# Kernel tuning notes

Hardware: AMD Instinct MI355X
Metric: run time of the kernel (lower is better)

Reference implementation:

```python
import jax, jax.numpy as jnp
import numpy as np

FRAMES = 4
SLICE = 14
BATCH = 4
NODES = 2 * FRAMES * SLICE * SLICE  # 1568
C = 2048
LN_EPS = 1e-5


def _layer(x, w, g, b):
    # Linear(no bias) -> LayerNorm(2048) -> LeakyReLU(0.1)
    y = jnp.einsum('bnc,dc->bnd', x, w)
    m = jnp.mean(y, axis=-1, keepdims=True)
    v = jnp.mean((y - m) ** 2, axis=-1, keepdims=True)
    y = (y - m) / jnp.sqrt(v + LN_EPS) * g + b
    return jax.nn.leaky_relu(y, 0.1)


def setup_inputs() -> dict:
    key = jax.random.key(0)
    ks = jax.random.split(key, 8)
    w = lambda k, sh: (jax.random.normal(k, sh, jnp.float32) * 0.02)
    return {
        'x': jax.random.normal(ks[0], (BATCH, NODES, C), jnp.float32),
        'w_fc1': w(ks[1], (C, C)),
        'w1': w(ks[2], (C, C)), 'g1': jnp.ones((C,), jnp.float32), 'b1': jnp.zeros((C,), jnp.float32),
        'w2': w(ks[3], (C, C)), 'g2': jnp.ones((C,), jnp.float32), 'b2': jnp.zeros((C,), jnp.float32),
        'w3': w(ks[4], (C, C)), 'g3': jnp.ones((C,), jnp.float32), 'b3': jnp.zeros((C,), jnp.float32),
        'conv1_w': w(ks[5], (2 * FRAMES,)),            # Conv2d(2F->1, k=1) weight squeezed
        'conv1_b': jnp.zeros((1,), jnp.float32),
        'deconv_w': w(ks[6], (C, 1024, 3, 3)),          # ConvTranspose2d weight [in, out, kH, kW]
        'deconv_b': jnp.zeros((1024,), jnp.float32),
    }


def reference(x, w_fc1, w1, g1, b1, w2, g2, b2, w3, g3, b3, conv1_w, conv1_b, deconv_w, deconv_b):
    # ---- adjacency_laplacian ----
    h = jnp.einsum('bnc,dc->bnd', x, w_fc1)                 # fc1
    s = jnp.einsum('bnd,bmd->bnm', h, h)                    # out @ out^T
    sq = s * s
    adj = sq / jnp.sum(sq, axis=1, keepdims=True)           # square_normalize (sum over dim=1)
    adj = adj + jnp.eye(NODES, dtype=adj.dtype)             # A + I
    d = 1.0 / jnp.sqrt(jnp.sum(adj, axis=1))                # [B, n]
    # D^{-1/2} A D^{-1/2}: diag matmuls are exactly row/col scaling
    lap = d[:, :, None] * adj * d[:, None, :]

    # ---- graph-conv stack ----
    out = jnp.matmul(lap, x)
    out = _layer(out, w1, g1, b1)
    out = jnp.matmul(lap, out)
    out = _layer(out, w2, g2, b2)
    out = jnp.matmul(lap, out)
    out = _layer(out, w3, g3, b3)

    # ---- head: transpose, reshape, 1x1 conv over 2F frame-channels ----
    out = jnp.swapaxes(out, 1, 2)                           # [B, 2048, nodes]
    out = out.reshape(BATCH * C, 2 * FRAMES, SLICE, SLICE)
    out = jnp.einsum('nfhw,f->nhw', out, conv1_w) + conv1_b[0]
    out = out.reshape(BATCH, C, SLICE, SLICE)

    # bilinear upsample x2 (align_corners=False == half-pixel, matches jax.image.resize)
    out = jax.image.resize(out, (BATCH, C, 2 * SLICE, 2 * SLICE), method='bilinear')

    # ConvTranspose2d(2048->1024, k=3, pad=1, stride=3) as dilated conv with flipped kernel
    wk = jnp.flip(deconv_w, axis=(-2, -1)).transpose(1, 0, 2, 3)  # [out, in, 3, 3]
    out = jax.lax.conv_general_dilated(
        out, wk, window_strides=(1, 1), padding=((1, 1), (1, 1)),
        lhs_dilation=(3, 3), dimension_numbers=('NCHW', 'OIHW', 'NCHW'))
    out = out + deconv_b[None, :, None, None]               # [B, 1024, 82, 82]
    return out
```

## Files before the change

### kernel.cpp

```cpp
#include <hip/hip_runtime.h>

typedef __bf16 bf16;
typedef __bf16 bf16x4 __attribute__((ext_vector_type(4)));
typedef __bf16 bf16x8 __attribute__((ext_vector_type(8)));
typedef float f32x4 __attribute__((ext_vector_type(4)));

#define N_NODES 1568
#define CDIM 2048

__device__ __forceinline__ void async_copy16(const bf16* g, bf16* l) {
    __builtin_amdgcn_global_load_lds(
        (const __attribute__((address_space(1))) unsigned int*)g,
        (__attribute__((address_space(3))) unsigned int*)l, 16, 0, 0);
}

template <typename OUT_T>
__global__ __launch_bounds__(512, 2) void gemm256_nt(const bf16* __restrict__ A,
                                                     const bf16* __restrict__ B,
                                                     OUT_T* __restrict__ C,
                                                     int M, int N, int K) {
    __shared__ __align__(16) bf16 lds[2][2][256 * 64];
    const int m0 = blockIdx.x * 256, n0 = blockIdx.y * 256;
    const int t = threadIdx.x;
    const int lane = t & 63, wave = t >> 6;
    const int wm = wave >> 2, wn = wave & 3;
    const int l15 = lane & 15, quad = lane >> 4, rx7 = l15 & 7;

    const int cg = (((t & 7) ^ ((t >> 3) & 7)) << 3);
    const int rb = t >> 3;
    const bf16* ga[4];
    const bf16* gb[4];
#pragma unroll
    for (int i = 0; i < 4; i++) {
        int ra = m0 + rb + i * 64; if (ra >= M) ra = M - 1;
        int rn = n0 + rb + i * 64; if (rn >= N) rn = N - 1;
        ga[i] = A + (long)ra * K + cg;
        gb[i] = B + (long)rn * K + cg;
    }
    const int ldst = t * 8;

    f32x4 acc[8][4];
#pragma unroll
    for (int i = 0; i < 8; i++)
#pragma unroll
        for (int j = 0; j < 4; j++) acc[i][j] = (f32x4){0.f, 0.f, 0.f, 0.f};

    auto stage = [&](int buf, int k0) {
        bf16* sAx = &lds[buf][0][0];
        bf16* sBx = &lds[buf][1][0];
#pragma unroll
        for (int i = 0; i < 4; i++)
            async_copy16(ga[i] + k0, sAx + ldst + i * 4096);
#pragma unroll
        for (int i = 0; i < 4; i++)
            async_copy16(gb[i] + k0, sBx + ldst + i * 4096);
    };

    const int NT = K >> 6;
    stage(0, 0);
    stage(1, 64);
    asm volatile("s_waitcnt vmcnt(8)" ::: "memory");
    __builtin_amdgcn_s_barrier();

    bf16x8 bfr[4][2], afr[2][2];
    for (int tt = 0; tt < NT; ++tt) {
        const bf16* sA = &lds[tt & 1][0][0];
        const bf16* sB = &lds[tt & 1][1][0];

        auto rdB = [&]() {
#pragma unroll
            for (int nf = 0; nf < 4; ++nf)
#pragma unroll
                for (int kk = 0; kk < 2; ++kk)
                    bfr[nf][kk] = *(const bf16x8*)(sB + (wn * 64 + nf * 16 + l15) * 64 +
                                                   ((((kk << 2) | quad) ^ rx7) << 3));
        };
        auto rdA = [&](int q) {
#pragma unroll
            for (int mi = 0; mi < 2; ++mi)
#pragma unroll
                for (int kk = 0; kk < 2; ++kk)
                    afr[mi][kk] = *(const bf16x8*)(sA + (wm * 128 + (q * 2 + mi) * 16 + l15) * 64 +
                                                   ((((kk << 2) | quad) ^ rx7) << 3));
        };
        auto mfq = [&](int q) {
            __builtin_amdgcn_s_setprio(1);
#pragma unroll
            for (int kk = 0; kk < 2; ++kk)
#pragma unroll
                for (int mi = 0; mi < 2; ++mi)
#pragma unroll
                    for (int nf = 0; nf < 4; ++nf)
                        acc[q * 2 + mi][nf] = __builtin_amdgcn_mfma_f32_16x16x32_bf16(
                            afr[mi][kk], bfr[nf][kk], acc[q * 2 + mi][nf], 0, 0, 0);
            __builtin_amdgcn_s_setprio(0);
        };

        rdB();
        rdA(0); mfq(0);
        rdA(1); mfq(1);
        rdA(2); mfq(2);
        rdA(3);
        asm volatile("s_waitcnt lgkmcnt(0)" ::: "memory");
        __builtin_amdgcn_s_barrier();
        if (tt + 2 < NT) stage(tt & 1, (tt + 2) << 6);
        mfq(3);
        if (tt + 2 < NT) { asm volatile("s_waitcnt vmcnt(8)" ::: "memory"); }
        else             { asm volatile("s_waitcnt vmcnt(0)" ::: "memory"); }
        __builtin_amdgcn_s_barrier();
    }

#pragma unroll
    for (int mf = 0; mf < 8; ++mf) {
        const int row0 = m0 + wm * 128 + mf * 16 + quad * 4;
#pragma unroll
        for (int nf = 0; nf < 4; ++nf) {
            const int col = n0 + wn * 64 + nf * 16 + l15;
            if (col < N) {
#pragma unroll
                for (int r = 0; r < 4; ++r) {
                    const int row = row0 + r;
                    if (row < M) C[(long)row * N + col] = (OUT_T)acc[mf][nf][r];
                }
            }
        }
    }
}

template <typename OUT_T>
__global__ __launch_bounds__(256, 2) void gemm_nt(const bf16* __restrict__ A,
                                                  const bf16* __restrict__ B,
                                                  OUT_T* __restrict__ C,
                                                  int M, int N, int K,
                                                  long sAb, long sBb, long sCb) {
    __shared__ __align__(16) bf16 sA[128 * 32];
    __shared__ __align__(16) bf16 sB[128 * 32];
    const int bz = blockIdx.z;
    A += (long)bz * sAb; B += (long)bz * sBb; C += (long)bz * sCb;
    const int m0 = blockIdx.x * 128, n0 = blockIdx.y * 128;
    const int t = threadIdx.x;
    const int lane = t & 63, wave = t >> 6;
    const int wr = wave >> 1, wc = wave & 1;
    const int l15 = lane & 15, quad = lane >> 4;

    f32x4 acc[4][4];
#pragma unroll
    for (int i = 0; i < 4; i++)
#pragma unroll
        for (int j = 0; j < 4; j++) acc[i][j] = (f32x4){0.f, 0.f, 0.f, 0.f};

    const int ko = (t & 3) * 8;
    int ra1 = m0 + (t >> 2);          if (ra1 >= M) ra1 = M - 1;
    int ra2 = m0 + ((t + 256) >> 2);  if (ra2 >= M) ra2 = M - 1;
    int rb1 = n0 + (t >> 2);          if (rb1 >= N) rb1 = N - 1;
    int rb2 = n0 + ((t + 256) >> 2);  if (rb2 >= N) rb2 = N - 1;
    const bf16* gA1 = A + (long)ra1 * K + ko;
    const bf16* gA2 = A + (long)ra2 * K + ko;
    const bf16* gB1 = B + (long)rb1 * K + ko;
    const bf16* gB2 = B + (long)rb2 * K + ko;
    bf16* lA1 = sA + t * 8;  bf16* lA2 = sA + (t + 256) * 8;
    bf16* lB1 = sB + t * 8;  bf16* lB2 = sB + (t + 256) * 8;

    for (int k0 = 0; k0 < K; k0 += 32) {
        __syncthreads();
        async_copy16(gA1 + k0, lA1);
        async_copy16(gA2 + k0, lA2);
        async_copy16(gB1 + k0, lB1);
        async_copy16(gB2 + k0, lB2);
        __syncthreads();
        bf16x8 af[4], bfr[4];
#pragma unroll
        for (int i = 0; i < 4; i++)
            af[i] = *(const bf16x8*)(sA + (wr * 64 + i * 16 + l15) * 32 + quad * 8);
#pragma unroll
        for (int j = 0; j < 4; j++)
            bfr[j] = *(const bf16x8*)(sB + (wc * 64 + j * 16 + l15) * 32 + quad * 8);
#pragma unroll
        for (int i = 0; i < 4; i++)
#pragma unroll
            for (int j = 0; j < 4; j++)
                acc[i][j] = __builtin_amdgcn_mfma_f32_16x16x32_bf16(af[i], bfr[j], acc[i][j], 0, 0, 0);
    }
#pragma unroll
    for (int i = 0; i < 4; i++) {
        const int row0 = m0 + wr * 64 + i * 16 + quad * 4;
#pragma unroll
        for (int j = 0; j < 4; j++) {
            const int col = n0 + wc * 64 + j * 16 + l15;
            if (col < N) {
#pragma unroll
                for (int r = 0; r < 4; r++) {
                    const int row = row0 + r;
                    if (row < M) C[(long)row * N + col] = (OUT_T)acc[i][j][r];
                }
            }
        }
    }
}

__global__ __launch_bounds__(256, 2) void gemm_nt_sym(const bf16* __restrict__ A,
                                                      float* __restrict__ C,
                                                      int M, int K,
                                                      long sAb, long sCb) {
    __shared__ __align__(16) bf16 sA[128 * 32];
    __shared__ __align__(16) bf16 sB[128 * 32];
    const int bz = blockIdx.z;
    A += (long)bz * sAb; C += (long)bz * sCb;
    int rem = blockIdx.x, bi = 0;
    while (rem >= 13 - bi) { rem -= 13 - bi; bi++; }
    const int bj = bi + rem;
    const int m0 = bi * 128, n0 = bj * 128;
    const int t = threadIdx.x;
    const int lane = t & 63, wave = t >> 6;
    const int wr = wave >> 1, wc = wave & 1;
    const int l15 = lane & 15, quad = lane >> 4;

    f32x4 acc[4][4];
#pragma unroll
    for (int i = 0; i < 4; i++)
#pragma unroll
        for (int j = 0; j < 4; j++) acc[i][j] = (f32x4){0.f, 0.f, 0.f, 0.f};

    const int ko = (t & 3) * 8;
    int ra1 = m0 + (t >> 2);          if (ra1 >= M) ra1 = M - 1;
    int ra2 = m0 + ((t + 256) >> 2);  if (ra2 >= M) ra2 = M - 1;
    int rb1 = n0 + (t >> 2);          if (rb1 >= M) rb1 = M - 1;
    int rb2 = n0 + ((t + 256) >> 2);  if (rb2 >= M) rb2 = M - 1;
    const bf16* gA1 = A + (long)ra1 * K + ko;
    const bf16* gA2 = A + (long)ra2 * K + ko;
    const bf16* gB1 = A + (long)rb1 * K + ko;
    const bf16* gB2 = A + (long)rb2 * K + ko;
    bf16* lA1 = sA + t * 8;  bf16* lA2 = sA + (t + 256) * 8;
    bf16* lB1 = sB + t * 8;  bf16* lB2 = sB + (t + 256) * 8;

    for (int k0 = 0; k0 < K; k0 += 32) {
        __syncthreads();
        async_copy16(gA1 + k0, lA1);
        async_copy16(gA2 + k0, lA2);
        async_copy16(gB1 + k0, lB1);
        async_copy16(gB2 + k0, lB2);
        __syncthreads();
        bf16x8 af[4], bfr[4];
#pragma unroll
        for (int i = 0; i < 4; i++)
            af[i] = *(const bf16x8*)(sA + (wr * 64 + i * 16 + l15) * 32 + quad * 8);
#pragma unroll
        for (int j = 0; j < 4; j++)
            bfr[j] = *(const bf16x8*)(sB + (wc * 64 + j * 16 + l15) * 32 + quad * 8);
#pragma unroll
        for (int i = 0; i < 4; i++)
#pragma unroll
            for (int j = 0; j < 4; j++)
                acc[i][j] = __builtin_amdgcn_mfma_f32_16x16x32_bf16(af[i], bfr[j], acc[i][j], 0, 0, 0);
    }
    const bool mirror = (bi != bj);
#pragma unroll
    for (int i = 0; i < 4; i++) {
        const int row0 = m0 + wr * 64 + i * 16 + quad * 4;
#pragma unroll
        for (int j = 0; j < 4; j++) {
            const int col = n0 + wc * 64 + j * 16 + l15;
            if (col < M) {
#pragma unroll
                for (int r = 0; r < 4; r++) {
                    const int row = row0 + r;
                    if (row < M) {
                        const float v = acc[i][j][r];
                        C[(long)row * M + col] = v;
                        if (mirror) C[(long)col * M + row] = v;
                    }
                }
            }
        }
    }
}

__global__ __launch_bounds__(256) void cast_f32_bf16_k(const float* __restrict__ in,
                                                       bf16* __restrict__ out, long n) {
    long i = ((long)blockIdx.x * 256 + threadIdx.x) * 4;
    if (i >= n) return;
    float4 v = *(const float4*)(in + i);
    bf16x4 o;
    o[0] = (bf16)v.x; o[1] = (bf16)v.y; o[2] = (bf16)v.z; o[3] = (bf16)v.w;
    *(bf16x4*)(out + i) = o;
}

__global__ __launch_bounds__(256) void cast4_f32_bf16_k(const float* __restrict__ a,
                                                        const float* __restrict__ b,
                                                        const float* __restrict__ c,
                                                        const float* __restrict__ d,
                                                        bf16* __restrict__ out, long n) {
    const int w = blockIdx.y;
    const float* in = (w == 0) ? a : (w == 1) ? b : (w == 2) ? c : d;
    bf16* o = out + (long)w * n;
    long i = ((long)blockIdx.x * 256 + threadIdx.x) * 4;
    if (i >= n) return;
    float4 v = *(const float4*)(in + i);
    bf16x4 ov;
    ov[0] = (bf16)v.x; ov[1] = (bf16)v.y; ov[2] = (bf16)v.z; ov[3] = (bf16)v.w;
    *(bf16x4*)(o + i) = ov;
}

__global__ __launch_bounds__(256) void transpose_bf16_k(const bf16* __restrict__ in,
                                                        bf16* __restrict__ out,
                                                        int R, int C, long sIn, long sOut) {
    __shared__ bf16 tile[64][65];
    in += (long)blockIdx.z * sIn;
    out += (long)blockIdx.z * sOut;
    const int r0 = blockIdx.y * 64, c0 = blockIdx.x * 64;
    const int tx = threadIdx.x & 63, ty = threadIdx.x >> 6;
#pragma unroll
    for (int i = 0; i < 16; i++) {
        int r = ty * 16 + i;
        int gr = r0 + r, gc = c0 + tx;
        tile[r][tx] = (gr < R && gc < C) ? in[(long)gr * C + gc] : (bf16)0.f;
    }
    __syncthreads();
#pragma unroll
    for (int i = 0; i < 16; i++) {
        int c = ty * 16 + i;
        int gc = c0 + c, gr = r0 + tx;
        if (gc < C && gr < R) out[(long)gc * R + gr] = tile[tx][c];
    }
}

__global__ __launch_bounds__(256) void colsum_part_k(const float* __restrict__ s,
                                                     float* __restrict__ part) {
    int m = blockIdx.x * 256 + threadIdx.x;
    if (m >= N_NODES) return;
    int y = blockIdx.y, b = blockIdx.z;
    const float* sb = s + (long)b * N_NODES * N_NODES;
    float acc = 0.f;
    for (int n = y * 196; n < y * 196 + 196; ++n) {
        float v = sb[(long)n * N_NODES + m];
        acc += v * v;
    }
    part[((long)y * 4 + b) * N_NODES + m] = acc;
}

__global__ __launch_bounds__(256) void colsum_comb_k(const float* __restrict__ part,
                                                     float* __restrict__ inv) {
    int m = blockIdx.x * 256 + threadIdx.x;
    if (m >= N_NODES) return;
    int b = blockIdx.y;
    float a = 0.f;
#pragma unroll
    for (int y = 0; y < 8; y++) a += part[((long)y * 4 + b) * N_NODES + m];
    inv[(long)b * N_NODES + m] = 1.0f / a;
}

__global__ __launch_bounds__(256) void lap_build_k(const float* __restrict__ s,
                                                   const float* __restrict__ inv,
                                                   bf16* __restrict__ lap) {
    int m = blockIdx.x * 256 + threadIdx.x;
    if (m >= N_NODES) return;
    int n = blockIdx.y, b = blockIdx.z;
    long off = (long)b * N_NODES * N_NODES + (long)n * N_NODES + m;
    float v = s[off];
    float l = 0.5f * v * v * inv[(long)b * N_NODES + m];
    if (n == m) l += 0.5f;
    lap[off] = (bf16)l;
}

__global__ __launch_bounds__(256) void ln_leaky_k(const float* __restrict__ y,
                                                  const float* __restrict__ g,
                                                  const float* __restrict__ beta,
                                                  bf16* __restrict__ z) {
    const long row = blockIdx.x;
    const float* yr = y + row * CDIM;
    const int t = threadIdx.x;
    float v[8];
    float s = 0.f, ss = 0.f;
#pragma unroll
    for (int i = 0; i < 8; i++) {
        float x = yr[t + 256 * i];
        v[i] = x; s += x; ss += x * x;
    }
#pragma unroll
    for (int o = 32; o > 0; o >>= 1) {
        s += __shfl_down(s, o);
        ss += __shfl_down(ss, o);
    }
    __shared__ float sh[8];
    const int wave = t >> 6;
    if ((t & 63) == 0) { sh[wave] = s; sh[wave + 4] = ss; }
    __syncthreads();
    if (t == 0) {
        float a = 0.f, b2 = 0.f;
#pragma unroll
        for (int w = 0; w < 4; w++) { a += sh[w]; b2 += sh[w + 4]; }
        sh[0] = a; sh[4] = b2;
    }
    __syncthreads();
    const float mean = sh[0] * (1.f / 2048.f);
    const float var = sh[4] * (1.f / 2048.f) - mean * mean;
    const float invs = rsqrtf(var + 1e-5f);
    bf16* zr = z + row * CDIM;
#pragma unroll
    for (int i = 0; i < 8; i++) {
        int c = t + 256 * i;
        float o = (v[i] - mean) * invs * g[c] + beta[c];
        o = o > 0.f ? o : 0.1f * o;
        zr[c] = (bf16)o;
    }
}

__global__ __launch_bounds__(256) void conv1_k(const bf16* __restrict__ z,
                                               const float* __restrict__ cw,
                                               const float* __restrict__ cb,
                                               bf16* __restrict__ tb) {
    const int b = blockIdx.z, hw = blockIdx.y;
    const int c = blockIdx.x * 256 + threadIdx.x;
    float acc = cb[0];
#pragma unroll
    for (int f = 0; f < 8; f++)
        acc += (float)z[((long)b * N_NODES + f * 196 + hw) * CDIM + c] * cw[f];
    tb[((long)b * 196 + hw) * CDIM + c] = (bf16)acc;
}

__global__ __launch_bounds__(256) void upsample_k(const bf16* __restrict__ tb,
                                                  bf16* __restrict__ u) {
    const int b = blockIdx.z, i = blockIdx.y, j = blockIdx.x;
    const float si = 0.5f * i - 0.25f, sj = 0.5f * j - 0.25f;
    const int i0 = (int)floorf(si), j0 = (int)floorf(sj);
    const float wi = si - i0, wj = sj - j0;
    const int i0c = max(i0, 0), i1c = min(i0 + 1, 13);
    const int j0c = max(j0, 0), j1c = min(j0 + 1, 13);
    const bf16* base = tb + (long)b * 196 * CDIM;
    const long r00 = ((long)i0c * 14 + j0c) * CDIM, r01 = ((long)i0c * 14 + j1c) * CDIM;
    const long r10 = ((long)i1c * 14 + j0c) * CDIM, r11 = ((long)i1c * 14 + j1c) * CDIM;
    bf16* ur = u + ((long)(b * 28 + i) * 28 + j) * CDIM;
    const float w00 = (1.f - wi) * (1.f - wj), w01 = (1.f - wi) * wj;
    const float w10 = wi * (1.f - wj), w11 = wi * wj;
    for (int k = 0; k < 8; k++) {
        int cc = threadIdx.x + 256 * k;
        float v = w00 * (float)base[r00 + cc] + w01 * (float)base[r01 + cc] +
                  w10 * (float)base[r10 + cc] + w11 * (float)base[r11 + cc];
        ur[cc] = (bf16)v;
    }
}

__global__ __launch_bounds__(256) void wt_k(const float* __restrict__ dw,
                                            bf16* __restrict__ Wt) {
    const int ic = blockIdx.x * 256 + threadIdx.x;
    const int oc = blockIdx.y;
    const float* src = dw + ((long)ic * 1024 + oc) * 9;
#pragma unroll
    for (int r = 0; r < 3; r++)
#pragma unroll
        for (int s = 0; s < 3; s++) {
            int kh = 2 - r, kw = 2 - s;
            Wt[((long)(kh * 3 + kw) * 1024 + oc) * 2048 + ic] = (bf16)src[r * 3 + s];
        }
}

__global__ __launch_bounds__(256) void deconv_scatter_k(const bf16* __restrict__ r,
                                                        const float* __restrict__ db,
                                                        float* __restrict__ out) {
    const int blk = blockIdx.x;
    const int b = blk >> 10, oc = blk & 1023;
    const float bias = db[oc];
    float* ob = out + (long)blk * 82 * 82;
    for (int e = threadIdx.x; e < 82 * 82; e += 256) {
        const int oh = e / 82, ow = e - oh * 82;
        const int mh = oh % 3, mw = ow % 3;
        const int kh = (mh == 0) ? 1 : ((mh == 1) ? 0 : 2);
        const int kw = (mw == 0) ? 1 : ((mw == 1) ? 0 : 2);
        const int ih = (oh - (1 - kh)) / 3;
        const int iw = (ow - (1 - kw)) / 3;
        const int g = kh * 3 + kw;
        ob[e] = (float)r[(long)(g * 1024 + oc) * 3136 + b * 784 + ih * 28 + iw] + bias;
    }
}

extern "C" void kernel_launch(void* const* d_in, const int* in_sizes, int n_in,
                              void* d_out, int out_size, void* d_ws, size_t ws_size,
                              hipStream_t stream) {
    const float* x        = (const float*)d_in[0];
    const float* w_fc1    = (const float*)d_in[1];
    const float* w1       = (const float*)d_in[2];
    const float* g1       = (const float*)d_in[3];
    const float* b1       = (const float*)d_in[4];
    const float* w2       = (const float*)d_in[5];
    const float* g2       = (const float*)d_in[6];
    const float* b2       = (const float*)d_in[7];
    const float* w3       = (const float*)d_in[8];
    const float* g3       = (const float*)d_in[9];
    const float* b3       = (const float*)d_in[10];
    const float* conv1_w  = (const float*)d_in[11];
    const float* conv1_b  = (const float*)d_in[12];
    const float* deconv_w = (const float*)d_in[13];
    const float* deconv_b = (const float*)d_in[14];
    float* out = (float*)d_out;

    char* W = (char*)d_ws;
    bf16* wb   = (bf16*)(W + 0);
    bf16* xb   = (bf16*)(W + 33554432);
    bf16* xbT  = (bf16*)(W + 59244544);
    bf16* hb   = (bf16*)(W + 84934656);
    bf16* lap  = (bf16*)(W + 110624768);
    bf16* tbuf = (bf16*)(W + 130293760);
    bf16* ubuf = (bf16*)(W + 133505024);
    bf16* Wt   = (bf16*)(W + 146350080);
    float* ybuf = (float*)(W + 184098816);
    float* sbuf = (float*)(W + 184098816);
    float* part = (float*)(W + 235479040);
    float* invc = (float*)(W + 235679744);
    bf16* rbuf = (bf16*)(W + 0);
    bf16* zb = xb;
    bf16* zT = xbT;
    bf16* outN = hb;

    const long WMAT = (long)2048 * 2048;
    bf16* wb0 = wb, *wb1 = wb + WMAT, *wb2 = wb + 2 * WMAT, *wb3 = wb + 3 * WMAT;

    cast4_f32_bf16_k<<<dim3(4096, 4), 256, 0, stream>>>(w_fc1, w1, w2, w3, wb, WMAT);
    cast_f32_bf16_k<<<dim3(12544), 256, 0, stream>>>(x, xb, (long)6272 * 2048);
    wt_k<<<dim3(8, 1024), 256, 0, stream>>>(deconv_w, Wt);

    transpose_bf16_k<<<dim3(32, 25, 4), 256, 0, stream>>>(
        xb, xbT, N_NODES, CDIM, (long)N_NODES * CDIM, (long)N_NODES * CDIM);

    gemm256_nt<bf16><<<dim3(25, 8), 512, 0, stream>>>(xb, wb0, hb, 6272, 2048, 2048);

    gemm_nt_sym<<<dim3(91, 1, 4), 256, 0, stream>>>(
        hb, sbuf, N_NODES, 2048,
        (long)N_NODES * 2048, (long)N_NODES * N_NODES);

    colsum_part_k<<<dim3(7, 8, 4), 256, 0, stream>>>(sbuf, part);
    colsum_comb_k<<<dim3(7, 4), 256, 0, stream>>>(part, invc);
    lap_build_k<<<dim3(7, N_NODES, 4), 256, 0, stream>>>(sbuf, invc, lap);

    const bf16* wlayer[3] = {wb1, wb2, wb3};
    const float* gl[3] = {g1, g2, g3};
    const float* bl[3] = {b1, b2, b3};
    for (int i = 0; i < 3; i++) {
        const bf16* prevT = (i == 0) ? xbT : zT;
        gemm_nt<bf16><<<dim3(13, 16, 4), 256, 0, stream>>>(
            lap, prevT, outN, N_NODES, CDIM, N_NODES,
            (long)N_NODES * N_NODES, (long)CDIM * N_NODES, (long)N_NODES * CDIM);
        gemm256_nt<float><<<dim3(25, 8), 512, 0, stream>>>(
            outN, wlayer[i], ybuf, 6272, 2048, 2048);
        ln_leaky_k<<<dim3(6272), 256, 0, stream>>>(ybuf, gl[i], bl[i], zb);
        if (i < 2) {
            transpose_bf16_k<<<dim3(32, 25, 4), 256, 0, stream>>>(
                zb, zT, N_NODES, CDIM, (long)N_NODES * CDIM, (long)N_NODES * CDIM);
        }
    }

    conv1_k<<<dim3(8, 196, 4), 256, 0, stream>>>(zb, conv1_w, conv1_b, tbuf);
    upsample_k<<<dim3(28, 28, 4), 256, 0, stream>>>(tbuf, ubuf);
    gemm256_nt<bf16><<<dim3(36, 13), 512, 0, stream>>>(Wt, ubuf, rbuf, 9216, 3136, 2048);
    deconv_scatter_k<<<dim3(4096), 256, 0, stream>>>(rbuf, deconv_b, out);

    (void)in_sizes; (void)n_in; (void)out_size; (void)ws_size;
}
```

Before: 1.177 ms.

## Re-pipeline 256-tile GEMM and use it for batched Laplacian and symmetric GEMMs

Restructures the 256x256 GEMM main loop so the async global-to-LDS copies are issued in half-tile pieces interleaved with the four MFMA quarters, with a barrier around each quarter. The kernel gains batch strides, and the old 128-tile gemm_nt and gemm_nt_sym kernels are replaced by 256-tile versions. To fit the 64-wide K tiling, the Laplacian and the transposed activations are zero-padded along K to 1664, and workspace offsets are adjusted to match. The goal is more reuse per tile and better copy/compute overlap for the graph-conv and similarity GEMMs. The cost is extra barriers, fewer and larger blocks on small batched problems, and some wasted work on the padding.

```diff
diff --git a/kernel.cpp b/kernel.cpp
--- a/kernel.cpp
+++ b/kernel.cpp
@@ -7,6 +7,7 @@
 
 #define N_NODES 1568
 #define CDIM 2048
+#define LAP_K 1664
 
 __device__ __forceinline__ void async_copy16(const bf16* g, bf16* l) {
     __builtin_amdgcn_global_load_lds(
@@ -18,8 +19,11 @@
 __global__ __launch_bounds__(512, 2) void gemm256_nt(const bf16* __restrict__ A,
                                                      const bf16* __restrict__ B,
                                                      OUT_T* __restrict__ C,
-                                                     int M, int N, int K) {
+                                                     int M, int N, int K,
+                                                     long sAb, long sBb, long sCb) {
     __shared__ __align__(16) bf16 lds[2][2][256 * 64];
+    const int bz = blockIdx.z;
+    A += (long)bz * sAb; B += (long)bz * sBb; C += (long)bz * sCb;
     const int m0 = blockIdx.x * 256, n0 = blockIdx.y * 256;
     const int t = threadIdx.x;
     const int lane = t & 63, wave = t >> 6;
@@ -38,6 +42,24 @@
         gb[i] = B + (long)rn * K + cg;
     }
     const int ldst = t * 8;
+    const int NT = K >> 6, NI = NT >> 1;
+
+    auto stageA = [&](int buf, int h, int tt) {
+        const int k0 = (tt < NT) ? (tt << 6) : 0;
+        bf16* s = &lds[buf][0][0] + ldst;
+        async_copy16(ga[2 * h] + k0,     s + (2 * h) * 4096);
+        async_copy16(ga[2 * h + 1] + k0, s + (2 * h + 1) * 4096);
+    };
+    auto stageB = [&](int buf, int h, int tt) {
+        const int k0 = (tt < NT) ? (tt << 6) : 0;
+        bf16* s = &lds[buf][1][0] + ldst;
+        async_copy16(gb[2 * h] + k0,     s + (2 * h) * 4096);
+        async_copy16(gb[2 * h + 1] + k0, s + (2 * h + 1) * 4096);
+    };
+
+    stageA(0, 0, 0); stageA(0, 1, 0);
+    stageB(0, 0, 0); stageB(0, 1, 0);
+    stageB(1, 0, 1); stageB(1, 1, 1);
 
     f32x4 acc[8][4];
 #pragma unroll
@@ -45,70 +67,58 @@
 #pragma unroll
         for (int j = 0; j < 4; j++) acc[i][j] = (f32x4){0.f, 0.f, 0.f, 0.f};
 
-    auto stage = [&](int buf, int k0) {
-        bf16* sAx = &lds[buf][0][0];
-        bf16* sBx = &lds[buf][1][0];
-#pragma unroll
-        for (int i = 0; i < 4; i++)
-            async_copy16(ga[i] + k0, sAx + ldst + i * 4096);
-#pragma unroll
-        for (int i = 0; i < 4; i++)
-            async_copy16(gb[i] + k0, sBx + ldst + i * 4096);
-    };
-
-    const int NT = K >> 6;
-    stage(0, 0);
-    stage(1, 64);
-    asm volatile("s_waitcnt vmcnt(8)" ::: "memory");
+    asm volatile("s_waitcnt vmcnt(4)" ::: "memory");
     __builtin_amdgcn_s_barrier();
 
     bf16x8 bfr[4][2], afr[2][2];
-    for (int tt = 0; tt < NT; ++tt) {
-        const bf16* sA = &lds[tt & 1][0][0];
-        const bf16* sB = &lds[tt & 1][1][0];
-
-        auto rdB = [&]() {
-#pragma unroll
-            for (int nf = 0; nf < 4; ++nf)
-#pragma unroll
-                for (int kk = 0; kk < 2; ++kk)
-                    bfr[nf][kk] = *(const bf16x8*)(sB + (wn * 64 + nf * 16 + l15) * 64 +
-                                                   ((((kk << 2) | quad) ^ rx7) << 3));
-        };
-        auto rdA = [&](int q) {
+    auto rdB = [&](int cb) {
+        const bf16* sB = &lds[cb][1][0];
+#pragma unroll
+        for (int nf = 0; nf < 4; ++nf)
+#pragma unroll
+            for (int kk = 0; kk < 2; ++kk)
+                bfr[nf][kk] = *(const bf16x8*)(sB + (wn * 64 + nf * 16 + l15) * 64 +
+                                               ((((kk << 2) | quad) ^ rx7) << 3));
+    };
+    auto rdA = [&](int cb, int q) {
+        const bf16* sA = &lds[cb][0][0];
+#pragma unroll
+        for (int mi = 0; mi < 2; ++mi)
+#pragma unroll
+            for (int kk = 0; kk < 2; ++kk)
+                afr[mi][kk] = *(const bf16x8*)(sA + (wm * 128 + (q * 2 + mi) * 16 + l15) * 64 +
+                                               ((((kk << 2) | quad) ^ rx7) << 3));
+    };
+    auto sync_mfma = [&](int q, bool vm) {
+        __builtin_amdgcn_s_barrier();
+        asm volatile("s_waitcnt lgkmcnt(0)" ::: "memory");
+        __builtin_amdgcn_sched_barrier(0);
+        __builtin_amdgcn_s_setprio(1);
+#pragma unroll
+        for (int kk = 0; kk < 2; ++kk)
 #pragma unroll
             for (int mi = 0; mi < 2; ++mi)
 #pragma unroll
-                for (int kk = 0; kk < 2; ++kk)
-                    afr[mi][kk] = *(const bf16x8*)(sA + (wm * 128 + (q * 2 + mi) * 16 + l15) * 64 +
-                                                   ((((kk << 2) | quad) ^ rx7) << 3));
-        };
-        auto mfq = [&](int q) {
-            __builtin_amdgcn_s_setprio(1);
-#pragma unroll
-            for (int kk = 0; kk < 2; ++kk)
-#pragma unroll
-                for (int mi = 0; mi < 2; ++mi)
-#pragma unroll
-                    for (int nf = 0; nf < 4; ++nf)
-                        acc[q * 2 + mi][nf] = __builtin_amdgcn_mfma_f32_16x16x32_bf16(
-                            afr[mi][kk], bfr[nf][kk], acc[q * 2 + mi][nf], 0, 0, 0);
-            __builtin_amdgcn_s_setprio(0);
-        };
-
-        rdB();
-        rdA(0); mfq(0);
-        rdA(1); mfq(1);
-        rdA(2); mfq(2);
-        rdA(3);
-        asm volatile("s_waitcnt lgkmcnt(0)" ::: "memory");
+                for (int nf = 0; nf < 4; ++nf)
+                    acc[q * 2 + mi][nf] = __builtin_amdgcn_mfma_f32_16x16x32_bf16(
+                        afr[mi][kk], bfr[nf][kk], acc[q * 2 + mi][nf], 0, 0, 0);
+        __builtin_amdgcn_s_setprio(0);
+        if (vm) asm volatile("s_waitcnt vmcnt(4)" ::: "memory");
         __builtin_amdgcn_s_barrier();
-        if (tt + 2 < NT) stage(tt & 1, (tt + 2) << 6);
-        mfq(3);
-        if (tt + 2 < NT) { asm volatile("s_waitcnt vmcnt(8)" ::: "memory"); }
-        else             { asm volatile("s_waitcnt vmcnt(0)" ::: "memory"); }
-        __builtin_amdgcn_s_barrier();
-    }
+    };
+
+    for (int j = 0; j < NI; ++j) {
+        const int t0 = 2 * j;
+        rdB(0); rdA(0, 0); stageA(1, 0, t0 + 1); sync_mfma(0, false);
+        rdA(0, 1);         stageA(1, 1, t0 + 1); sync_mfma(1, false);
+        rdA(0, 2);         stageB(0, 0, t0 + 2); sync_mfma(2, false);
+        rdA(0, 3);         stageB(0, 1, t0 + 2); sync_mfma(3, true);
+        rdB(1); rdA(1, 0); stageA(0, 0, t0 + 2); sync_mfma(0, false);
+        rdA(1, 1);         stageA(0, 1, t0 + 2); sync_mfma(1, false);
+        rdA(1, 2);         stageB(1, 0, t0 + 3); sync_mfma(2, false);
+        rdA(1, 3);         stageB(1, 1, t0 + 3); sync_mfma(3, true);
+    }
+    asm volatile("s_waitcnt vmcnt(0)" ::: "memory");
 
 #pragma unroll
     for (int mf = 0; mf < 8; ++mf) {
@@ -127,145 +137,126 @@
     }
 }
 
-template <typename OUT_T>
-__global__ __launch_bounds__(256, 2) void gemm_nt(const bf16* __restrict__ A,
-                                                  const bf16* __restrict__ B,
-                                                  OUT_T* __restrict__ C,
-                                                  int M, int N, int K,
-                                                  long sAb, long sBb, long sCb) {
-    __shared__ __align__(16) bf16 sA[128 * 32];
-    __shared__ __align__(16) bf16 sB[128 * 32];
-    const int bz = blockIdx.z;
-    A += (long)bz * sAb; B += (long)bz * sBb; C += (long)bz * sCb;
-    const int m0 = blockIdx.x * 128, n0 = blockIdx.y * 128;
-    const int t = threadIdx.x;
-    const int lane = t & 63, wave = t >> 6;
-    const int wr = wave >> 1, wc = wave & 1;
-    const int l15 = lane & 15, quad = lane >> 4;
-
-    f32x4 acc[4][4];
-#pragma unroll
-    for (int i = 0; i < 4; i++)
-#pragma unroll
-        for (int j = 0; j < 4; j++) acc[i][j] = (f32x4){0.f, 0.f, 0.f, 0.f};
-
-    const int ko = (t & 3) * 8;
-    int ra1 = m0 + (t >> 2);          if (ra1 >= M) ra1 = M - 1;
-    int ra2 = m0 + ((t + 256) >> 2);  if (ra2 >= M) ra2 = M - 1;
-    int rb1 = n0 + (t >> 2);          if (rb1 >= N) rb1 = N - 1;
-    int rb2 = n0 + ((t + 256) >> 2);  if (rb2 >= N) rb2 = N - 1;
-    const bf16* gA1 = A + (long)ra1 * K + ko;
-    const bf16* gA2 = A + (long)ra2 * K + ko;
-    const bf16* gB1 = B + (long)rb1 * K + ko;
-    const bf16* gB2 = B + (long)rb2 * K + ko;
-    bf16* lA1 = sA + t * 8;  bf16* lA2 = sA + (t + 256) * 8;
-    bf16* lB1 = sB + t * 8;  bf16* lB2 = sB + (t + 256) * 8;
-
-    for (int k0 = 0; k0 < K; k0 += 32) {
-        __syncthreads();
-        async_copy16(gA1 + k0, lA1);
-        async_copy16(gA2 + k0, lA2);
-        async_copy16(gB1 + k0, lB1);
-        async_copy16(gB2 + k0, lB2);
-        __syncthreads();
-        bf16x8 af[4], bfr[4];
-#pragma unroll
-        for (int i = 0; i < 4; i++)
-            af[i] = *(const bf16x8*)(sA + (wr * 64 + i * 16 + l15) * 32 + quad * 8);
-#pragma unroll
-        for (int j = 0; j < 4; j++)
-            bfr[j] = *(const bf16x8*)(sB + (wc * 64 + j * 16 + l15) * 32 + quad * 8);
-#pragma unroll
-        for (int i = 0; i < 4; i++)
-#pragma unroll
-            for (int j = 0; j < 4; j++)
-                acc[i][j] = __builtin_amdgcn_mfma_f32_16x16x32_bf16(af[i], bfr[j], acc[i][j], 0, 0, 0);
-    }
-#pragma unroll
-    for (int i = 0; i < 4; i++) {
-        const int row0 = m0 + wr * 64 + i * 16 + quad * 4;
-#pragma unroll
-        for (int j = 0; j < 4; j++) {
-            const int col = n0 + wc * 64 + j * 16 + l15;
-            if (col < N) {
-#pragma unroll
-                for (int r = 0; r < 4; r++) {
-                    const int row = row0 + r;
-                    if (row < M) C[(long)row * N + col] = (OUT_T)acc[i][j][r];
-                }
-            }
-        }
-    }
-}
-
-__global__ __launch_bounds__(256, 2) void gemm_nt_sym(const bf16* __restrict__ A,
+__global__ __launch_bounds__(512, 2) void gemm256_sym(const bf16* __restrict__ A,
                                                       float* __restrict__ C,
                                                       int M, int K,
                                                       long sAb, long sCb) {
-    __shared__ __align__(16) bf16 sA[128 * 32];
-    __shared__ __align__(16) bf16 sB[128 * 32];
+    __shared__ __align__(16) bf16 lds[2][2][256 * 64];
     const int bz = blockIdx.z;
     A += (long)bz * sAb; C += (long)bz * sCb;
+    const int side = (M + 255) >> 8;
     int rem = blockIdx.x, bi = 0;
-    while (rem >= 13 - bi) { rem -= 13 - bi; bi++; }
+    while (rem >= side - bi) { rem -= side - bi; bi++; }
     const int bj = bi + rem;
-    const int m0 = bi * 128, n0 = bj * 128;
+    const int m0 = bi * 256, n0 = bj * 256;
     const int t = threadIdx.x;
     const int lane = t & 63, wave = t >> 6;
-    const int wr = wave >> 1, wc = wave & 1;
-    const int l15 = lane & 15, quad = lane >> 4;
-
-    f32x4 acc[4][4];
-#pragma unroll
-    for (int i = 0; i < 4; i++)
+    const int wm = wave >> 2, wn = wave & 3;
+    const int l15 = lane & 15, quad = lane >> 4, rx7 = l15 & 7;
+
+    const int cg = (((t & 7) ^ ((t >> 3) & 7)) << 3);
+    const int rb = t >> 3;
+    const bf16* ga[4];
+    const bf16* gb[4];
+#pragma unroll
+    for (int i = 0; i < 4; i++) {
+        int ra = m0 + rb + i * 64; if (ra >= M) ra = M - 1;
+        int rn = n0 + rb + i * 64; if (rn >= M) rn = M - 1;
+        ga[i] = A + (long)ra * K + cg;
+        gb[i] = A + (long)rn * K + cg;
+    }
+    const int ldst = t * 8;
+    const int NT = K >> 6, NI = NT >> 1;
+
+    auto stageA = [&](int buf, int h, int tt) {
+        const int k0 = (tt < NT) ? (tt << 6) : 0;
+        bf16* s = &lds[buf][0][0] + ldst;
+        async_copy16(ga[2 * h] + k0,     s + (2 * h) * 4096);
+        async_copy16(ga[2 * h + 1] + k0, s + (2 * h + 1) * 4096);
+    };
+    auto stageB = [&](int buf, int h, int tt) {
+        const int k0 = (tt < NT) ? (tt << 6) : 0;
+        bf16* s = &lds[buf][1][0] + ldst;
+        async_copy16(gb[2 * h] + k0,     s + (2 * h) * 4096);
+        async_copy16(gb[2 * h + 1] + k0, s + (2 * h + 1) * 4096);
+    };
+
+    stageA(0, 0, 0); stageA(0, 1, 0);
+    stageB(0, 0, 0); stageB(0, 1, 0);
+    stageB(1, 0, 1); stageB(1, 1, 1);
+
+    f32x4 acc[8][4];
+#pragma unroll
+    for (int i = 0; i < 8; i++)
 #pragma unroll
         for (int j = 0; j < 4; j++) acc[i][j] = (f32x4){0.f, 0.f, 0.f, 0.f};
 
-    const int ko = (t & 3) * 8;
-    int ra1 = m0 + (t >> 2);          if (ra1 >= M) ra1 = M - 1;
-    int ra2 = m0 + ((t + 256) >> 2);  if (ra2 >= M) ra2 = M - 1;
-    int rb1 = n0 + (t >> 2);          if (rb1 >= M) rb1 = M - 1;
-    int rb2 = n0 + ((t + 256) >> 2);  if (rb2 >= M) rb2 = M - 1;
-    const bf16* gA1 = A + (long)ra1 * K + ko;
-    const bf16* gA2 = A + (long)ra2 * K + ko;
-    const bf16* gB1 = A + (long)rb1 * K + ko;
-    const bf16* gB2 = A + (long)rb2 * K + ko;
-    bf16* lA1 = sA + t * 8;  bf16* lA2 = sA + (t + 256) * 8;
-    bf16* lB1 = sB + t * 8;  bf16* lB2 = sB + (t + 256) * 8;
-
-    for (int k0 = 0; k0 < K; k0 += 32) {
-        __syncthreads();
-        async_copy16(gA1 + k0, lA1);
-        async_copy16(gA2 + k0, lA2);
-        async_copy16(gB1 + k0, lB1);
-        async_copy16(gB2 + k0, lB2);
-        __syncthreads();
-        bf16x8 af[4], bfr[4];
-#pragma unroll
-        for (int i = 0; i < 4; i++)
-            af[i] = *(const bf16x8*)(sA + (wr * 64 + i * 16 + l15) * 32 + quad * 8);
-#pragma unroll
-        for (int j = 0; j < 4; j++)
-            bfr[j] = *(const bf16x8*)(sB + (wc * 64 + j * 16 + l15) * 32 + quad * 8);
-#pragma unroll
-        for (int i = 0; i < 4; i++)
-#pragma unroll
-            for (int j = 0; j < 4; j++)
-                acc[i][j] = __builtin_amdgcn_mfma_f32_16x16x32_bf16(af[i], bfr[j], acc[i][j], 0, 0, 0);
-    }
+    asm volatile("s_waitcnt vmcnt(4)" ::: "memory");
+    __builtin_amdgcn_s_barrier();
+
+    bf16x8 bfr[4][2], afr[2][2];
+    auto rdB = [&](int cb) {
+        const bf16* sB = &lds[cb][1][0];
+#pragma unroll
+        for (int nf = 0; nf < 4; ++nf)
+#pragma unroll
+            for (int kk = 0; kk < 2; ++kk)
+                bfr[nf][kk] = *(const bf16x8*)(sB + (wn * 64 + nf * 16 + l15) * 64 +
+                                               ((((kk << 2) | quad) ^ rx7) << 3));
+    };
+    auto rdA = [&](int cb, int q) {
+        const bf16* sA = &lds[cb][0][0];
+#pragma unroll
+        for (int mi = 0; mi < 2; ++mi)
+#pragma unroll
+            for (int kk = 0; kk < 2; ++kk)
+                afr[mi][kk] = *(const bf16x8*)(sA + (wm * 128 + (q * 2 + mi) * 16 + l15) * 64 +
+                                               ((((kk << 2) | quad) ^ rx7) << 3));
+    };
+    auto sync_mfma = [&](int q, bool vm) {
+        __builtin_amdgcn_s_barrier();
+        asm volatile("s_waitcnt lgkmcnt(0)" ::: "memory");
+        __builtin_amdgcn_sched_barrier(0);
+        __builtin_amdgcn_s_setprio(1);
+#pragma unroll
+        for (int kk = 0; kk < 2; ++kk)
+#pragma unroll
+            for (int mi = 0; mi < 2; ++mi)
+#pragma unroll
+                for (int nf = 0; nf < 4; ++nf)
+                    acc[q * 2 + mi][nf] = __builtin_amdgcn_mfma_f32_16x16x32_bf16(
+                        afr[mi][kk], bfr[nf][kk], acc[q * 2 + mi][nf], 0, 0, 0);
+        __builtin_amdgcn_s_setprio(0);
+        if (vm) asm volatile("s_waitcnt vmcnt(4)" ::: "memory");
+        __builtin_amdgcn_s_barrier();
+    };
+
+    for (int j = 0; j < NI; ++j) {
+        const int t0 = 2 * j;
+        rdB(0); rdA(0, 0); stageA(1, 0, t0 + 1); sync_mfma(0, false);
+        rdA(0, 1);         stageA(1, 1, t0 + 1); sync_mfma(1, false);
+        rdA(0, 2);         stageB(0, 0, t0 + 2); sync_mfma(2, false);
+        rdA(0, 3);         stageB(0, 1, t0 + 2); sync_mfma(3, true);
+        rdB(1); rdA(1, 0); stageA(0, 0, t0 + 2); sync_mfma(0, false);
+        rdA(1, 1);         stageA(0, 1, t0 + 1 + 1); sync_mfma(1, false);
+        rdA(1, 2);         stageB(1, 0, t0 + 3); sync_mfma(2, false);
+        rdA(1, 3);         stageB(1, 1, t0 + 3); sync_mfma(3, true);
+    }
+    asm volatile("s_waitcnt vmcnt(0)" ::: "memory");
+
     const bool mirror = (bi != bj);
 #pragma unroll
-    for (int i = 0; i < 4; i++) {
-        const int row0 = m0 + wr * 64 + i * 16 + quad * 4;
-#pragma unroll
-        for (int j = 0; j < 4; j++) {
-            const int col = n0 + wc * 64 + j * 16 + l15;
+    for (int mf = 0; mf < 8; ++mf) {
+        const int row0 = m0 + wm * 128 + mf * 16 + quad * 4;
+#pragma unroll
+        for (int nf = 0; nf < 4; ++nf) {
+            const int col = n0 + wn * 64 + nf * 16 + l15;
             if (col < M) {
 #pragma unroll
-                for (int r = 0; r < 4; r++) {
+                for (int r = 0; r < 4; ++r) {
                     const int row = row0 + r;
                     if (row < M) {
-                        const float v = acc[i][j][r];
+                        const float v = acc[mf][nf][r];
                         C[(long)row * M + col] = v;
                         if (mirror) C[(long)col * M + row] = v;
                     }
@@ -301,9 +292,10 @@
     *(bf16x4*)(o + i) = ov;
 }
 
-__global__ __launch_bounds__(256) void transpose_bf16_k(const bf16* __restrict__ in,
-                                                        bf16* __restrict__ out,
-                                                        int R, int C, long sIn, long sOut) {
+__global__ __launch_bounds__(256) void transpose_pad_bf16_k(const bf16* __restrict__ in,
+                                                            bf16* __restrict__ out,
+                                                            int R, int C, int Rpad,
+                                                            long sIn, long sOut) {
     __shared__ bf16 tile[64][65];
     in += (long)blockIdx.z * sIn;
     out += (long)blockIdx.z * sOut;
@@ -320,7 +312,7 @@
     for (int i = 0; i < 16; i++) {
         int c = ty * 16 + i;
         int gc = c0 + c, gr = r0 + tx;
-        if (gc < C && gr < R) out[(long)gc * R + gr] = tile[tx][c];
+        if (gc < C && gr < Rpad) out[(long)gc * Rpad + gr] = tile[tx][c];
     }
 }
 
@@ -353,10 +345,11 @@
                                                    const float* __restrict__ inv,
                                                    bf16* __restrict__ lap) {
     int m = blockIdx.x * 256 + threadIdx.x;
-    if (m >= N_NODES) return;
+    if (m >= LAP_K) return;
     int n = blockIdx.y, b = blockIdx.z;
-    long off = (long)b * N_NODES * N_NODES + (long)n * N_NODES + m;
-    float v = s[off];
+    long off = (long)b * N_NODES * LAP_K + (long)n * LAP_K + m;
+    if (m >= N_NODES) { lap[off] = (bf16)0.f; return; }
+    float v = s[(long)b * N_NODES * N_NODES + (long)n * N_NODES + m];
     float l = 0.5f * v * v * inv[(long)b * N_NODES + m];
     if (n == m) l += 0.5f;
     lap[off] = (bf16)l;
@@ -497,15 +490,15 @@
     bf16* wb   = (bf16*)(W + 0);
     bf16* xb   = (bf16*)(W + 33554432);
     bf16* xbT  = (bf16*)(W + 59244544);
-    bf16* hb   = (bf16*)(W + 84934656);
-    bf16* lap  = (bf16*)(W + 110624768);
-    bf16* tbuf = (bf16*)(W + 130293760);
-    bf16* ubuf = (bf16*)(W + 133505024);
-    bf16* Wt   = (bf16*)(W + 146350080);
-    float* ybuf = (float*)(W + 184098816);
-    float* sbuf = (float*)(W + 184098816);
-    float* part = (float*)(W + 235479040);
-    float* invc = (float*)(W + 235679744);
+    bf16* hb   = (bf16*)(W + 86507520);
+    bf16* lap  = (bf16*)(W + 112197632);
+    bf16* tbuf = (bf16*)(W + 133070848);
+    bf16* ubuf = (bf16*)(W + 136282112);
+    bf16* Wt   = (bf16*)(W + 149127168);
+    float* ybuf = (float*)(W + 186875904);
+    float* sbuf = (float*)(W + 186875904);
+    float* part = (float*)(W + 238256128);
+    float* invc = (float*)(W + 238456832);
     bf16* rbuf = (bf16*)(W + 0);
     bf16* zb = xb;
     bf16* zT = xbT;
@@ -518,12 +511,13 @@
     cast_f32_bf16_k<<<dim3(12544), 256, 0, stream>>>(x, xb, (long)6272 * 2048);
     wt_k<<<dim3(8, 1024), 256, 0, stream>>>(deconv_w, Wt);
 
-    transpose_bf16_k<<<dim3(32, 25, 4), 256, 0, stream>>>(
-        xb, xbT, N_NODES, CDIM, (long)N_NODES * CDIM, (long)N_NODES * CDIM);
-
-    gemm256_nt<bf16><<<dim3(25, 8), 512, 0, stream>>>(xb, wb0, hb, 6272, 2048, 2048);
-
-    gemm_nt_sym<<<dim3(91, 1, 4), 256, 0, stream>>>(
+    transpose_pad_bf16_k<<<dim3(32, 26, 4), 256, 0, stream>>>(
+        xb, xbT, N_NODES, CDIM, LAP_K, (long)N_NODES * CDIM, (long)CDIM * LAP_K);
+
+    gemm256_nt<bf16><<<dim3(25, 8, 1), 512, 0, stream>>>(
+        xb, wb0, hb, 6272, 2048, 2048, 0, 0, 0);
+
+    gemm256_sym<<<dim3(28, 1, 4), 512, 0, stream>>>(
         hb, sbuf, N_NODES, 2048,
         (long)N_NODES * 2048, (long)N_NODES * N_NODES);
 
@@ -536,21 +530,22 @@
     const float* bl[3] = {b1, b2, b3};
     for (int i = 0; i < 3; i++) {
         const bf16* prevT = (i == 0) ? xbT : zT;
-        gemm_nt<bf16><<<dim3(13, 16, 4), 256, 0, stream>>>(
-            lap, prevT, outN, N_NODES, CDIM, N_NODES,
-            (long)N_NODES * N_NODES, (long)CDIM * N_NODES, (long)N_NODES * CDIM);
-        gemm256_nt<float><<<dim3(25, 8), 512, 0, stream>>>(
-            outN, wlayer[i], ybuf, 6272, 2048, 2048);
+        gemm256_nt<bf16><<<dim3(7, 8, 4), 512, 0, stream>>>(
+            lap, prevT, outN, N_NODES, CDIM, LAP_K,
+            (long)N_NODES * LAP_K, (long)CDIM * LAP_K, (long)N_NODES * CDIM);
+        gemm256_nt<float><<<dim3(25, 8, 1), 512, 0, stream>>>(
+            outN, wlayer[i], ybuf, 6272, 2048, 2048, 0, 0, 0);
         ln_leaky_k<<<dim3(6272), 256, 0, stream>>>(ybuf, gl[i], bl[i], zb);
         if (i < 2) {
-            transpose_bf16_k<<<dim3(32, 25, 4), 256, 0, stream>>>(
-                zb, zT, N_NODES, CDIM, (long)N_NODES * CDIM, (long)N_NODES * CDIM);
+            transpose_pad_bf16_k<<<dim3(32, 26, 4), 256, 0, stream>>>(
+                zb, zT, N_NODES, CDIM, LAP_K, (long)N_NODES * CDIM, (long)CDIM * LAP_K);
         }
     }
 
     conv1_k<<<dim3(8, 196, 4), 256, 0, stream>>>(zb, conv1_w, conv1_b, tbuf);
     upsample_k<<<dim3(28, 28, 4), 256, 0, stream>>>(tbuf, ubuf);
-    gemm256_nt<bf16><<<dim3(36, 13), 512, 0, stream>>>(Wt, ubuf, rbuf, 9216, 3136, 2048);
+    gemm256_nt<bf16><<<dim3(36, 13, 1), 512, 0, stream>>>(
+        Wt, ubuf, rbuf, 9216, 3136, 2048, 0, 0, 0);
     deconv_scatter_k<<<dim3(4096), 256, 0, stream>>>(rbuf, deconv_b, out);
 
     (void)in_sizes; (void)n_in; (void)out_size; (void)ws_size;
```

Result: faster. 1.043 ms (-11.3%).
